# Performance work log

Measured on AMD Instinct MI355X. Metric: run time of the kernel, lower is better.

## Reference

```python
import jax, jax.numpy as jnp
import numpy as np

N_SRC1, N_TGT1, N_TGT2 = 200000, 50000, 10000
E1, E2 = 1000000, 300000
F_IN, F_HID, F_OUT = 256, 192, 128


def setup_inputs() -> dict:
    key = jax.random.key(0)
    ks = jax.random.split(key, 16)
    x = jax.random.normal(ks[0], (N_SRC1, F_IN), dtype=jnp.float32)
    ei1 = jnp.stack([
        jax.random.randint(ks[1], (E1,), 0, N_SRC1, dtype=jnp.int32),
        jax.random.randint(ks[2], (E1,), 0, N_TGT1, dtype=jnp.int32),
    ])
    ei2 = jnp.stack([
        jax.random.randint(ks[3], (E2,), 0, N_TGT1, dtype=jnp.int32),
        jax.random.randint(ks[4], (E2,), 0, N_TGT2, dtype=jnp.int32),
    ])
    def w(k, o, i):
        return jax.random.normal(k, (o, i), dtype=jnp.float32) * (1.0 / np.sqrt(i))
    return {
        "x": x, "ei1": ei1, "ei2": ei2,
        "Wl1": w(ks[5], F_HID, F_IN), "bl1": jnp.zeros((F_HID,), jnp.float32), "Wr1": w(ks[6], F_HID, F_IN),
        "Wl2": w(ks[7], F_HID, F_HID), "bl2": jnp.zeros((F_HID,), jnp.float32), "Wr2": w(ks[8], F_HID, F_HID),
        "W1": w(ks[9], F_HID, F_HID), "b1": jnp.zeros((F_HID,), jnp.float32),
        "W2": w(ks[10], F_OUT, F_HID), "b2": jnp.zeros((F_OUT,), jnp.float32),
    }


def _segment_mean(feat, tgt, n):
    s = jax.ops.segment_sum(feat, tgt, num_segments=n)  # [n, d]
    c = jax.ops.segment_sum(jnp.ones((tgt.shape[0], 1), feat.dtype), tgt, num_segments=n)
    return s / jnp.maximum(c, 1.0)


def _sage_conv(x, ei, n_tgt, Wl, bl, Wr):
    # PyG SAGEConv (mean aggr): lin_l(mean of src feats per tgt) + lin_r(x_target)
    agg = _segment_mean(x[ei[0]], ei[1], n_tgt)
    return agg @ Wl.T + bl + x[:n_tgt] @ Wr.T


def reference(x, ei1, ei2, Wl1, bl1, Wr1, Wl2, bl2, Wr2, W1, b1, W2, b2):
    h = jax.nn.relu(_sage_conv(x, ei1, N_TGT1, Wl1, bl1, Wr1))   # dropout is identity in eval
    h = jax.nn.relu(_sage_conv(h, ei2, N_TGT2, Wl2, bl2, Wr2))
    embedding = h @ W1.T + b1
    h = jax.nn.relu(embedding)
    logits = h @ W2.T + b2
    return jax.nn.log_softmax(logits, axis=-1), embedding
```

## Files before the change

### kernel.cpp

```cpp
#include <hip/hip_runtime.h>
#include <hip/hip_bf16.h>

#define N_SRC1 200000
#define N_TGT1 50000
#define N_TGT2 10000
#define E1_N   1000000
#define E2_N   300000
#define F_IN   256
#define F_HID  192
#define F_OUT  128

typedef __attribute__((ext_vector_type(4))) float f32x4;
typedef __attribute__((ext_vector_type(8))) short short8;

__device__ inline float bf2f(ushort u) {
    union { uint i; float f; } c; c.i = ((uint)u) << 16; return c.f;
}
__device__ inline ushort f2bf(float f) {
    union { float f; uint i; } c; c.f = f;
    uint u = c.i;
    return (ushort)((u + 0x7FFFu + ((u >> 16) & 1u)) >> 16);
}
__device__ inline uint pack2(float a, float b) {
    return (uint)f2bf(a) | ((uint)f2bf(b) << 16);
}

__global__ __launch_bounds__(256) void prep(
    const float4* __restrict__ x4, uint2* __restrict__ xb,
    const float* __restrict__ Wl1, const float* __restrict__ Wr1,
    const float* __restrict__ Wl2, const float* __restrict__ Wr2,
    const float* __restrict__ W1, const float* __restrict__ W2,
    ushort* __restrict__ wc1, ushort* __restrict__ wc2,
    ushort* __restrict__ w1b, ushort* __restrict__ w2b)
{
    const int b = blockIdx.x, tid = threadIdx.x;
    if (b < 2048) {
        const int n4 = N_SRC1 * F_IN / 4;
        for (int i = b * 256 + tid; i < n4; i += 2048 * 256) {
            float4 v = x4[i];
            uint2 o;
            o.x = pack2(v.x, v.y);
            o.y = pack2(v.z, v.w);
            xb[i] = o;
        }
        return;
    }
    const int wt = (b - 2048) * 256 + tid;
    for (int idx = wt; idx < 233472; idx += 128 * 256) {
        if (idx < 98304) {
            int n = idx >> 9, k = idx & 511;
            float v = (k < 256) ? Wl1[n * 256 + k] : Wr1[n * 256 + (k - 256)];
            wc1[idx] = f2bf(v);
        } else if (idx < 98304 + 73728) {
            int i2 = idx - 98304;
            int n = i2 / 384, k = i2 - n * 384;
            float v = (k < 192) ? Wl2[n * 192 + k] : Wr2[n * 192 + (k - 192)];
            wc2[i2] = f2bf(v);
        } else if (idx < 98304 + 73728 + 36864) {
            int i3 = idx - (98304 + 73728);
            w1b[i3] = f2bf(W1[i3]);
        } else {
            int i4 = idx - (98304 + 73728 + 36864);
            w2b[i4] = f2bf(W2[i4]);
        }
    }
}

__global__ __launch_bounds__(256) void hist_kernel(
    const int* __restrict__ tgt, int* __restrict__ cnt, int E)
{
    int i = blockIdx.x * blockDim.x + threadIdx.x;
    if (i < E) atomicAdd(cnt + tgt[i], 1);
}

__global__ __launch_bounds__(256) void scan_blocks(
    const int* __restrict__ cnt, int n, int* __restrict__ off,
    int* __restrict__ partials)
{
    __shared__ int s[256];
    int tid = threadIdx.x;
    int i = blockIdx.x * 256 + tid;
    int v = (i < n) ? cnt[i] : 0;
    s[tid] = v;
    __syncthreads();
#pragma unroll
    for (int o = 1; o < 256; o <<= 1) {
        int t = (tid >= o) ? s[tid - o] : 0;
        __syncthreads();
        s[tid] += t;
        __syncthreads();
    }
    if (i < n) off[i] = s[tid] - v;
    if (tid == 255) partials[blockIdx.x] = s[255];
}

__global__ __launch_bounds__(256) void scan_partials_block(
    int* __restrict__ partials, int np, int* __restrict__ total_out)
{
    __shared__ int s[256];
    int tid = threadIdx.x;
    int v = (tid < np) ? partials[tid] : 0;
    s[tid] = v;
    __syncthreads();
#pragma unroll
    for (int o = 1; o < 256; o <<= 1) {
        int t = (tid >= o) ? s[tid - o] : 0;
        __syncthreads();
        s[tid] += t;
        __syncthreads();
    }
    if (tid < np) partials[tid] = s[tid] - v;
    if (tid == 255) *total_out = s[255];
}

__global__ __launch_bounds__(256) void add_off(
    int* __restrict__ off, const int* __restrict__ partials,
    int* __restrict__ cur, int n)
{
    int i = blockIdx.x * blockDim.x + threadIdx.x;
    if (i < n) {
        int v = off[i] + partials[i >> 8];
        off[i] = v;
        cur[i] = v;
    }
}

__global__ __launch_bounds__(256) void fill_edges(
    const int* __restrict__ src, const int* __restrict__ tgt,
    int* __restrict__ cur, int* __restrict__ esrc, int E)
{
    int i = blockIdx.x * blockDim.x + threadIdx.x;
    if (i < E) {
        int pos = atomicAdd(cur + tgt[i], 1);
        esrc[pos] = src[i];
    }
}

__global__ __launch_bounds__(256) void aggregate_bf16_256(
    const int* __restrict__ esrc, const int* __restrict__ off,
    const ushort* __restrict__ X, ushort* __restrict__ seg, int n)
{
    int wid  = blockIdx.x * 4 + (threadIdx.x >> 6);
    int lane = threadIdx.x & 63;
    if (wid >= n) return;
    int s0 = off[wid], s1 = off[wid + 1];
    float a0 = 0, a1 = 0, a2 = 0, a3 = 0;
    const uint2* base = (const uint2*)X;
    int e = s0;
    for (; e + 4 <= s1; e += 4) {
        int i0 = esrc[e], i1 = esrc[e + 1], i2 = esrc[e + 2], i3 = esrc[e + 3];
        uint2 v0 = base[(size_t)i0 * 64 + lane];
        uint2 v1 = base[(size_t)i1 * 64 + lane];
        uint2 v2 = base[(size_t)i2 * 64 + lane];
        uint2 v3 = base[(size_t)i3 * 64 + lane];
        a0 += bf2f((ushort)(v0.x & 0xffff)) + bf2f((ushort)(v1.x & 0xffff))
            + bf2f((ushort)(v2.x & 0xffff)) + bf2f((ushort)(v3.x & 0xffff));
        a1 += bf2f((ushort)(v0.x >> 16)) + bf2f((ushort)(v1.x >> 16))
            + bf2f((ushort)(v2.x >> 16)) + bf2f((ushort)(v3.x >> 16));
        a2 += bf2f((ushort)(v0.y & 0xffff)) + bf2f((ushort)(v1.y & 0xffff))
            + bf2f((ushort)(v2.y & 0xffff)) + bf2f((ushort)(v3.y & 0xffff));
        a3 += bf2f((ushort)(v0.y >> 16)) + bf2f((ushort)(v1.y >> 16))
            + bf2f((ushort)(v2.y >> 16)) + bf2f((ushort)(v3.y >> 16));
    }
    for (; e < s1; ++e) {
        uint2 v = base[(size_t)esrc[e] * 64 + lane];
        a0 += bf2f((ushort)(v.x & 0xffff)); a1 += bf2f((ushort)(v.x >> 16));
        a2 += bf2f((ushort)(v.y & 0xffff)); a3 += bf2f((ushort)(v.y >> 16));
    }
    float inv = (s1 > s0) ? 1.0f / (float)(s1 - s0) : 0.0f;
    uint2 o;
    o.x = pack2(a0 * inv, a1 * inv);
    o.y = pack2(a2 * inv, a3 * inv);
    ((uint2*)seg)[(size_t)wid * 64 + lane] = o;
}

__global__ __launch_bounds__(256) void aggregate_bf16_192(
    const int* __restrict__ esrc, const int* __restrict__ off,
    const ushort* __restrict__ X, ushort* __restrict__ seg, int n)
{
    int wid  = blockIdx.x * 4 + (threadIdx.x >> 6);
    int lane = threadIdx.x & 63;
    if (wid >= n) return;
    int s0 = off[wid], s1 = off[wid + 1];
    float a0 = 0, a1 = 0, a2 = 0, a3 = 0;
    const uint* base = (const uint*)X;
    int e = s0;
    for (; e + 4 <= s1; e += 4) {
        const uint* r0 = base + (size_t)esrc[e] * 96;
        const uint* r1 = base + (size_t)esrc[e + 1] * 96;
        const uint* r2 = base + (size_t)esrc[e + 2] * 96;
        const uint* r3 = base + (size_t)esrc[e + 3] * 96;
        uint w0 = r0[lane], w1 = r1[lane], w2 = r2[lane], w3 = r3[lane];
        a0 += bf2f((ushort)(w0 & 0xffff)) + bf2f((ushort)(w1 & 0xffff))
            + bf2f((ushort)(w2 & 0xffff)) + bf2f((ushort)(w3 & 0xffff));
        a1 += bf2f((ushort)(w0 >> 16)) + bf2f((ushort)(w1 >> 16))
            + bf2f((ushort)(w2 >> 16)) + bf2f((ushort)(w3 >> 16));
        if (lane < 32) {
            uint u0 = r0[64 + lane], u1 = r1[64 + lane],
                 u2 = r2[64 + lane], u3 = r3[64 + lane];
            a2 += bf2f((ushort)(u0 & 0xffff)) + bf2f((ushort)(u1 & 0xffff))
                + bf2f((ushort)(u2 & 0xffff)) + bf2f((ushort)(u3 & 0xffff));
            a3 += bf2f((ushort)(u0 >> 16)) + bf2f((ushort)(u1 >> 16))
                + bf2f((ushort)(u2 >> 16)) + bf2f((ushort)(u3 >> 16));
        }
    }
    for (; e < s1; ++e) {
        const uint* r = base + (size_t)esrc[e] * 96;
        uint v0 = r[lane];
        a0 += bf2f((ushort)(v0 & 0xffff)); a1 += bf2f((ushort)(v0 >> 16));
        if (lane < 32) {
            uint v1 = r[64 + lane];
            a2 += bf2f((ushort)(v1 & 0xffff)); a3 += bf2f((ushort)(v1 >> 16));
        }
    }
    float inv = (s1 > s0) ? 1.0f / (float)(s1 - s0) : 0.0f;
    uint* o = (uint*)seg + (size_t)wid * 96;
    o[lane] = pack2(a0 * inv, a1 * inv);
    if (lane < 32) o[64 + lane] = pack2(a2 * inv, a3 * inv);
}

template <int BM, int BN, int WM, int WN>
__global__ __launch_bounds__(WM * WN * 64) void gemm_mfma(
    const ushort* __restrict__ A1, int K1,
    const ushort* __restrict__ A2, int K2,
    const ushort* __restrict__ W, const float* __restrict__ bias,
    ushort* __restrict__ Cb, float* __restrict__ Cf,
    int M, int relu)
{
    constexpr int TPB = WM * WN * 64;
    constexpr int WTM = BM / WM, WTN = BN / WN;
    constexpr int MF = WTM / 16, NF = WTN / 16;
    constexpr int ROW = 40;
    __shared__ __attribute__((aligned(16))) ushort As[BM * ROW];
    __shared__ __attribute__((aligned(16))) ushort Ws[BN * ROW];
    const int tid  = threadIdx.x;
    const int lane = tid & 63;
    const int wid  = tid >> 6;
    const int wm = wid / WN, wn = wid % WN;
    const int bm = blockIdx.x * BM;
    const int K = K1 + K2;

    f32x4 acc[MF][NF];
#pragma unroll
    for (int i = 0; i < MF; ++i)
#pragma unroll
        for (int j = 0; j < NF; ++j) acc[i][j] = {0.f, 0.f, 0.f, 0.f};

    for (int k0 = 0; k0 < K; k0 += 32) {
#pragma unroll
        for (int c = tid; c < BM * 4; c += TPB) {
            int row = c >> 2, k8 = (c & 3) * 8;
            int m = bm + row, k = k0 + k8;
            uint4 v = make_uint4(0, 0, 0, 0);
            if (m < M) {
                const ushort* s = (k < K1) ? (A1 + (size_t)m * K1 + k)
                                           : (A2 + (size_t)m * K2 + (k - K1));
                v = *(const uint4*)s;
            }
            *(uint4*)&As[row * ROW + k8] = v;
        }
#pragma unroll
        for (int c = tid; c < BN * 4; c += TPB) {
            int row = c >> 2, k8 = (c & 3) * 8;
            uint4 v = *(const uint4*)(W + (size_t)row * K + k0 + k8);
            *(uint4*)&Ws[row * ROW + k8] = v;
        }
        __syncthreads();
        short8 a[MF], b[NF];
#pragma unroll
        for (int mf = 0; mf < MF; ++mf)
            a[mf] = *(const short8*)&As[(wm * WTM + mf * 16 + (lane & 15)) * ROW + (lane >> 4) * 8];
#pragma unroll
        for (int nf = 0; nf < NF; ++nf)
            b[nf] = *(const short8*)&Ws[(wn * WTN + nf * 16 + (lane & 15)) * ROW + (lane >> 4) * 8];
#pragma unroll
        for (int mf = 0; mf < MF; ++mf)
#pragma unroll
            for (int nf = 0; nf < NF; ++nf)
                acc[mf][nf] = __builtin_amdgcn_mfma_f32_16x16x32_bf16(
                    a[mf], b[nf], acc[mf][nf], 0, 0, 0);
        __syncthreads();
    }

#pragma unroll
    for (int mf = 0; mf < MF; ++mf) {
        int r0 = bm + wm * WTM + mf * 16 + (lane >> 4) * 4;
#pragma unroll
        for (int nf = 0; nf < NF; ++nf) {
            int cc = wn * WTN + nf * 16 + (lane & 15);
            float bi = bias[cc];
#pragma unroll
            for (int r = 0; r < 4; ++r) {
                int m = r0 + r;
                if (m >= M) continue;
                float v = acc[mf][nf][r] + bi;
                if (Cf) Cf[(size_t)m * BN + cc] = v;
                if (Cb) Cb[(size_t)m * BN + cc] = f2bf(relu ? fmaxf(v, 0.f) : v);
            }
        }
    }
}

__global__ __launch_bounds__(256) void logsoftmax128(
    const float* __restrict__ logits, float* __restrict__ out, int M)
{
    long long gid = (long long)blockIdx.x * blockDim.x + threadIdx.x;
    int row  = (int)(gid >> 6);
    int lane = (int)(gid & 63);
    if (row >= M) return;
    const float* r = logits + (size_t)row * 128;
    float a = r[lane], b = r[lane + 64];
    float mx = fmaxf(a, b);
#pragma unroll
    for (int o = 32; o > 0; o >>= 1) mx = fmaxf(mx, __shfl_xor(mx, o));
    float s = expf(a - mx) + expf(b - mx);
#pragma unroll
    for (int o = 32; o > 0; o >>= 1) s += __shfl_xor(s, o);
    float ls = logf(s) + mx;
    out[(size_t)row * 128 + lane]      = a - ls;
    out[(size_t)row * 128 + lane + 64] = b - ls;
}

extern "C" void kernel_launch(void* const* d_in, const int* in_sizes, int n_in,
                              void* d_out, int out_size, void* d_ws, size_t ws_size,
                              hipStream_t stream)
{
    const float* x   = (const float*)d_in[0];
    const int*   ei1 = (const int*)d_in[1];
    const int*   ei2 = (const int*)d_in[2];
    const float* Wl1 = (const float*)d_in[3];
    const float* bl1 = (const float*)d_in[4];
    const float* Wr1 = (const float*)d_in[5];
    const float* Wl2 = (const float*)d_in[6];
    const float* bl2 = (const float*)d_in[7];
    const float* Wr2 = (const float*)d_in[8];
    const float* W1  = (const float*)d_in[9];
    const float* b1  = (const float*)d_in[10];
    const float* W2  = (const float*)d_in[11];
    const float* b2  = (const float*)d_in[12];

    char* ws = (char*)d_ws;
    ushort* xb    = (ushort*)(ws + 0);
    ushort* seg1b = (ushort*)(ws + 102400000);
    ushort* h1b   = (ushort*)(ws + 128000000);
    int*    esrc1 = (int*)   (ws + 147200000);
    int*    cnt1  = (int*)   (ws + 151200000);
    int*    off1  = (int*)   (ws + 151400000);
    int*    part  = (int*)   (ws + 151600064);
    ushort* wc1   = (ushort*)(ws + 151601152);
    ushort* wc2   = (ushort*)(ws + 151797760);
    ushort* w1b   = (ushort*)(ws + 151945216);
    ushort* w2b   = (ushort*)(ws + 152018944);
    ushort* seg2b = (ushort*)(ws + 152068096);
    int*    esrc2 = (int*)   (ws + 147200000);
    int*    cnt2  = (int*)   (ws + 148400000);
    int*    off2  = (int*)   (ws + 148440064);
    ushort* h2b    = (ushort*)(ws + 102400000);
    ushort* h3b    = (ushort*)(ws + 106240000);
    float*  logits = (float*) (ws + 110080000);

    float* out_ls  = (float*)d_out;
    float* out_emb = (float*)d_out + (size_t)N_TGT2 * F_OUT;

    const int NP1 = (N_TGT1 + 255) / 256;
    const int NP2 = (N_TGT2 + 255) / 256;

    prep<<<2176, 256, 0, stream>>>(
        (const float4*)x, (uint2*)xb, Wl1, Wr1, Wl2, Wr2, W1, W2,
        wc1, wc2, w1b, w2b);

    hipMemsetAsync(cnt1, 0, 200000, stream);
    hist_kernel<<<(E1_N + 255) / 256, 256, 0, stream>>>(ei1 + E1_N, cnt1, E1_N);
    scan_blocks<<<NP1, 256, 0, stream>>>(cnt1, N_TGT1, off1, part);
    scan_partials_block<<<1, 256, 0, stream>>>(part, NP1, off1 + N_TGT1);
    add_off<<<NP1, 256, 0, stream>>>(off1, part, cnt1 , N_TGT1);
    fill_edges<<<(E1_N + 255) / 256, 256, 0, stream>>>(ei1, ei1 + E1_N, cnt1, esrc1, E1_N);
    aggregate_bf16_256<<<(N_TGT1 + 3) / 4, 256, 0, stream>>>(esrc1, off1, xb, seg1b, N_TGT1);

    gemm_mfma<128, 192, 4, 2><<<(N_TGT1 + 127) / 128, 512, 0, stream>>>(
        seg1b, F_IN, xb, F_IN, wc1, bl1, h1b, nullptr, N_TGT1, 1);

    hipMemsetAsync(cnt2, 0, 40000, stream);
    hist_kernel<<<(E2_N + 255) / 256, 256, 0, stream>>>(ei2 + E2_N, cnt2, E2_N);
    scan_blocks<<<NP2, 256, 0, stream>>>(cnt2, N_TGT2, off2, part);
    scan_partials_block<<<1, 256, 0, stream>>>(part, NP2, off2 + N_TGT2);
    add_off<<<NP2, 256, 0, stream>>>(off2, part, cnt2 , N_TGT2);
    fill_edges<<<(E2_N + 255) / 256, 256, 0, stream>>>(ei2, ei2 + E2_N, cnt2, esrc2, E2_N);
    aggregate_bf16_192<<<(N_TGT2 + 3) / 4, 256, 0, stream>>>(esrc2, off2, h1b, seg2b, N_TGT2);

    gemm_mfma<64, 192, 4, 2><<<(N_TGT2 + 63) / 64, 512, 0, stream>>>(
        seg2b, F_HID, h1b, F_HID, wc2, bl2, h2b, nullptr, N_TGT2, 1);

    gemm_mfma<64, 192, 4, 2><<<(N_TGT2 + 63) / 64, 512, 0, stream>>>(
        h2b, F_HID, nullptr, 0, w1b, b1, h3b, out_emb, N_TGT2, 1);

    gemm_mfma<64, 128, 4, 2><<<(N_TGT2 + 63) / 64, 512, 0, stream>>>(
        h3b, F_HID, nullptr, 0, w2b, b2, nullptr, logits, N_TGT2, 0);

    logsoftmax128<<<(N_TGT2 * 64 + 255) / 256, 256, 0, stream>>>(logits, out_ls, N_TGT2);
}
```

Before: 396.5 us.

## Fuse histograms into prep, single-block scans, fuse tail GEMMs with log-softmax

Both edge histograms now run inside the prep kernel. The multi-kernel prefix scans are replaced by one 1024-thread scan kernel per layer. The layer-2 SAGE GEMM, the embedding GEMM, the output GEMM and log-softmax are fused into one kernel that keeps the intermediates in LDS. The aggregation loop is unrolled to 8 gathers, and the layer-1 GEMM tile changes to 64x192 with a 2x4 wave grid. Together these remove about ten launches and the global round-trips of the tail intermediates. The costs are a single-block serial scan and a tail kernel with large LDS use and low occupancy.

```diff
diff --git a/kernel.cpp b/kernel.cpp
--- a/kernel.cpp
+++ b/kernel.cpp
@@ -25,13 +25,18 @@
     return (uint)f2bf(a) | ((uint)f2bf(b) << 16);
 }
 
+#define HB1 3907
+#define HB2 1172
+
 __global__ __launch_bounds__(256) void prep(
     const float4* __restrict__ x4, uint2* __restrict__ xb,
     const float* __restrict__ Wl1, const float* __restrict__ Wr1,
     const float* __restrict__ Wl2, const float* __restrict__ Wr2,
     const float* __restrict__ W1, const float* __restrict__ W2,
     ushort* __restrict__ wc1, ushort* __restrict__ wc2,
-    ushort* __restrict__ w1b, ushort* __restrict__ w2b)
+    ushort* __restrict__ w1b, ushort* __restrict__ w2b,
+    const int* __restrict__ tgt1, const int* __restrict__ tgt2,
+    int* __restrict__ cnt1, int* __restrict__ cnt2)
 {
     const int b = blockIdx.x, tid = threadIdx.x;
     if (b < 2048) {
@@ -45,84 +50,65 @@
         }
         return;
     }
-    const int wt = (b - 2048) * 256 + tid;
-    for (int idx = wt; idx < 233472; idx += 128 * 256) {
-        if (idx < 98304) {
-            int n = idx >> 9, k = idx & 511;
-            float v = (k < 256) ? Wl1[n * 256 + k] : Wr1[n * 256 + (k - 256)];
-            wc1[idx] = f2bf(v);
-        } else if (idx < 98304 + 73728) {
-            int i2 = idx - 98304;
-            int n = i2 / 384, k = i2 - n * 384;
-            float v = (k < 192) ? Wl2[n * 192 + k] : Wr2[n * 192 + (k - 192)];
-            wc2[i2] = f2bf(v);
-        } else if (idx < 98304 + 73728 + 36864) {
-            int i3 = idx - (98304 + 73728);
-            w1b[i3] = f2bf(W1[i3]);
-        } else {
-            int i4 = idx - (98304 + 73728 + 36864);
-            w2b[i4] = f2bf(W2[i4]);
-        }
-    }
-}
-
-__global__ __launch_bounds__(256) void hist_kernel(
-    const int* __restrict__ tgt, int* __restrict__ cnt, int E)
-{
-    int i = blockIdx.x * blockDim.x + threadIdx.x;
-    if (i < E) atomicAdd(cnt + tgt[i], 1);
-}
-
-__global__ __launch_bounds__(256) void scan_blocks(
-    const int* __restrict__ cnt, int n, int* __restrict__ off,
-    int* __restrict__ partials)
-{
-    __shared__ int s[256];
-    int tid = threadIdx.x;
-    int i = blockIdx.x * 256 + tid;
-    int v = (i < n) ? cnt[i] : 0;
-    s[tid] = v;
+    if (b < 2176) {
+        const int wt = (b - 2048) * 256 + tid;
+        for (int idx = wt; idx < 233472; idx += 128 * 256) {
+            if (idx < 98304) {
+                int n = idx >> 9, k = idx & 511;
+                float v = (k < 256) ? Wl1[n * 256 + k] : Wr1[n * 256 + (k - 256)];
+                wc1[idx] = f2bf(v);
+            } else if (idx < 98304 + 73728) {
+                int i2 = idx - 98304;
+                int n = i2 / 384, k = i2 - n * 384;
+                float v = (k < 192) ? Wl2[n * 192 + k] : Wr2[n * 192 + (k - 192)];
+                wc2[i2] = f2bf(v);
+            } else if (idx < 98304 + 73728 + 36864) {
+                int i3 = idx - (98304 + 73728);
+                w1b[i3] = f2bf(W1[i3]);
+            } else {
+                int i4 = idx - (98304 + 73728 + 36864);
+                w2b[i4] = f2bf(W2[i4]);
+            }
+        }
+        return;
+    }
+    if (b < 2176 + HB1) {
+        int e = (b - 2176) * 256 + tid;
+        if (e < E1_N) atomicAdd(cnt1 + tgt1[e], 1);
+        return;
+    }
+    int e = (b - 2176 - HB1) * 256 + tid;
+    if (e < E2_N) atomicAdd(cnt2 + tgt2[e], 1);
+}
+
+__global__ __launch_bounds__(1024) void scan_full(
+    int* __restrict__ cnt, int n, int* __restrict__ off)
+{
+    __shared__ int s[1024];
+    const int tid = threadIdx.x;
+    const int chunk = (n + 1023) >> 10;
+    int lo = tid * chunk, hi = lo + chunk;
+    if (lo > n) lo = n;
+    if (hi > n) hi = n;
+    int sum = 0;
+    for (int i = lo; i < hi; ++i) sum += cnt[i];
+    s[tid] = sum;
     __syncthreads();
 #pragma unroll
-    for (int o = 1; o < 256; o <<= 1) {
+    for (int o = 1; o < 1024; o <<= 1) {
         int t = (tid >= o) ? s[tid - o] : 0;
         __syncthreads();
         s[tid] += t;
         __syncthreads();
     }
-    if (i < n) off[i] = s[tid] - v;
-    if (tid == 255) partials[blockIdx.x] = s[255];
-}
-
-__global__ __launch_bounds__(256) void scan_partials_block(
-    int* __restrict__ partials, int np, int* __restrict__ total_out)
-{
-    __shared__ int s[256];
-    int tid = threadIdx.x;
-    int v = (tid < np) ? partials[tid] : 0;
-    s[tid] = v;
-    __syncthreads();
-#pragma unroll
-    for (int o = 1; o < 256; o <<= 1) {
-        int t = (tid >= o) ? s[tid - o] : 0;
-        __syncthreads();
-        s[tid] += t;
-        __syncthreads();
-    }
-    if (tid < np) partials[tid] = s[tid] - v;
-    if (tid == 255) *total_out = s[255];
-}
-
-__global__ __launch_bounds__(256) void add_off(
-    int* __restrict__ off, const int* __restrict__ partials,
-    int* __restrict__ cur, int n)
-{
-    int i = blockIdx.x * blockDim.x + threadIdx.x;
-    if (i < n) {
-        int v = off[i] + partials[i >> 8];
-        off[i] = v;
-        cur[i] = v;
-    }
+    int run = s[tid] - sum;
+    for (int i = lo; i < hi; ++i) {
+        int v = cnt[i];
+        off[i] = run;
+        cnt[i] = run;
+        run += v;
+    }
+    if (tid == 1023) off[n] = s[1023];
 }
 
 __global__ __launch_bounds__(256) void fill_edges(
@@ -147,20 +133,18 @@
     float a0 = 0, a1 = 0, a2 = 0, a3 = 0;
     const uint2* base = (const uint2*)X;
     int e = s0;
-    for (; e + 4 <= s1; e += 4) {
-        int i0 = esrc[e], i1 = esrc[e + 1], i2 = esrc[e + 2], i3 = esrc[e + 3];
-        uint2 v0 = base[(size_t)i0 * 64 + lane];
-        uint2 v1 = base[(size_t)i1 * 64 + lane];
-        uint2 v2 = base[(size_t)i2 * 64 + lane];
-        uint2 v3 = base[(size_t)i3 * 64 + lane];
-        a0 += bf2f((ushort)(v0.x & 0xffff)) + bf2f((ushort)(v1.x & 0xffff))
-            + bf2f((ushort)(v2.x & 0xffff)) + bf2f((ushort)(v3.x & 0xffff));
-        a1 += bf2f((ushort)(v0.x >> 16)) + bf2f((ushort)(v1.x >> 16))
-            + bf2f((ushort)(v2.x >> 16)) + bf2f((ushort)(v3.x >> 16));
-        a2 += bf2f((ushort)(v0.y & 0xffff)) + bf2f((ushort)(v1.y & 0xffff))
-            + bf2f((ushort)(v2.y & 0xffff)) + bf2f((ushort)(v3.y & 0xffff));
-        a3 += bf2f((ushort)(v0.y >> 16)) + bf2f((ushort)(v1.y >> 16))
-            + bf2f((ushort)(v2.y >> 16)) + bf2f((ushort)(v3.y >> 16));
+    for (; e + 8 <= s1; e += 8) {
+        uint2 v[8];
+#pragma unroll
+        for (int j = 0; j < 8; ++j)
+            v[j] = base[(size_t)esrc[e + j] * 64 + lane];
+#pragma unroll
+        for (int j = 0; j < 8; ++j) {
+            a0 += bf2f((ushort)(v[j].x & 0xffff));
+            a1 += bf2f((ushort)(v[j].x >> 16));
+            a2 += bf2f((ushort)(v[j].y & 0xffff));
+            a3 += bf2f((ushort)(v[j].y >> 16));
+        }
     }
     for (; e < s1; ++e) {
         uint2 v = base[(size_t)esrc[e] * 64 + lane];
@@ -224,8 +208,7 @@
     const ushort* __restrict__ A1, int K1,
     const ushort* __restrict__ A2, int K2,
     const ushort* __restrict__ W, const float* __restrict__ bias,
-    ushort* __restrict__ Cb, float* __restrict__ Cf,
-    int M, int relu)
+    ushort* __restrict__ Cb, int M, int relu)
 {
     constexpr int TPB = WM * WN * 64;
     constexpr int WTM = BM / WM, WTN = BN / WN;
@@ -294,31 +277,158 @@
                 int m = r0 + r;
                 if (m >= M) continue;
                 float v = acc[mf][nf][r] + bi;
-                if (Cf) Cf[(size_t)m * BN + cc] = v;
-                if (Cb) Cb[(size_t)m * BN + cc] = f2bf(relu ? fmaxf(v, 0.f) : v);
-            }
-        }
-    }
-}
-
-__global__ __launch_bounds__(256) void logsoftmax128(
-    const float* __restrict__ logits, float* __restrict__ out, int M)
-{
-    long long gid = (long long)blockIdx.x * blockDim.x + threadIdx.x;
-    int row  = (int)(gid >> 6);
-    int lane = (int)(gid & 63);
-    if (row >= M) return;
-    const float* r = logits + (size_t)row * 128;
-    float a = r[lane], b = r[lane + 64];
-    float mx = fmaxf(a, b);
-#pragma unroll
-    for (int o = 32; o > 0; o >>= 1) mx = fmaxf(mx, __shfl_xor(mx, o));
-    float s = expf(a - mx) + expf(b - mx);
-#pragma unroll
-    for (int o = 32; o > 0; o >>= 1) s += __shfl_xor(s, o);
-    float ls = logf(s) + mx;
-    out[(size_t)row * 128 + lane]      = a - ls;
-    out[(size_t)row * 128 + lane + 64] = b - ls;
+                Cb[(size_t)m * BN + cc] = f2bf(relu ? fmaxf(v, 0.f) : v);
+            }
+        }
+    }
+}
+
+__global__ __launch_bounds__(512) void tail_fused(
+    const ushort* __restrict__ seg2, const ushort* __restrict__ h1,
+    const ushort* __restrict__ wc2, const float* __restrict__ bl2,
+    const ushort* __restrict__ w1b, const float* __restrict__ b1,
+    const ushort* __restrict__ w2b, const float* __restrict__ b2,
+    float* __restrict__ out_emb, float* __restrict__ out_ls, int M)
+{
+    __shared__ __attribute__((aligned(16))) char lds[122880];
+    ushort* As0   = (ushort*)lds;
+    ushort* Ws0   = (ushort*)(lds + 5120);
+    ushort* h2buf = (ushort*)(lds + 20480);
+    ushort* h3buf = (ushort*)(lds + 46080);
+    ushort* w2buf = (ushort*)(lds + 71680);
+    float*  lsbuf = (float*)(lds + 71680);
+
+    const int tid = threadIdx.x, lane = tid & 63, wid = tid >> 6;
+    const int wm = wid >> 1, wn = wid & 1;
+    const int bm = blockIdx.x * 64;
+
+    for (int c = tid; c < 128 * 24; c += 512) {
+        int r = c / 24, k8 = (c % 24) * 8;
+        uint4 v = *(const uint4*)(w2b + r * 192 + k8);
+        *(uint4*)&w2buf[r * 200 + k8] = v;
+    }
+
+    {
+        f32x4 acc[6];
+#pragma unroll
+        for (int j = 0; j < 6; ++j) acc[j] = {0.f, 0.f, 0.f, 0.f};
+        for (int k0 = 0; k0 < 384; k0 += 32) {
+            if (tid < 256) {
+                int row = tid >> 2, k8 = (tid & 3) * 8;
+                int m = bm + row, k = k0 + k8;
+                uint4 v = make_uint4(0, 0, 0, 0);
+                if (m < M) {
+                    const ushort* s = (k < 192) ? (seg2 + (size_t)m * 192 + k)
+                                                : (h1 + (size_t)m * 192 + (k - 192));
+                    v = *(const uint4*)s;
+                }
+                *(uint4*)&As0[row * 40 + k8] = v;
+            }
+            for (int c = tid; c < 768; c += 512) {
+                int row = c >> 2, k8 = (c & 3) * 8;
+                uint4 v = *(const uint4*)(wc2 + (size_t)row * 384 + k0 + k8);
+                *(uint4*)&Ws0[row * 40 + k8] = v;
+            }
+            __syncthreads();
+            short8 a = *(const short8*)&As0[(wm * 16 + (lane & 15)) * 40 + (lane >> 4) * 8];
+#pragma unroll
+            for (int nf = 0; nf < 6; ++nf) {
+                short8 b = *(const short8*)&Ws0[(wn * 96 + nf * 16 + (lane & 15)) * 40 + (lane >> 4) * 8];
+                acc[nf] = __builtin_amdgcn_mfma_f32_16x16x32_bf16(a, b, acc[nf], 0, 0, 0);
+            }
+            __syncthreads();
+        }
+#pragma unroll
+        for (int nf = 0; nf < 6; ++nf) {
+            int cc = wn * 96 + nf * 16 + (lane & 15);
+            float bi = bl2[cc];
+#pragma unroll
+            for (int r = 0; r < 4; ++r) {
+                int row = wm * 16 + (lane >> 4) * 4 + r;
+                h2buf[row * 200 + cc] = f2bf(fmaxf(acc[nf][r] + bi, 0.f));
+            }
+        }
+    }
+    __syncthreads();
+
+    {
+        f32x4 acc[6];
+#pragma unroll
+        for (int j = 0; j < 6; ++j) acc[j] = {0.f, 0.f, 0.f, 0.f};
+        for (int k0 = 0; k0 < 192; k0 += 32) {
+            for (int c = tid; c < 768; c += 512) {
+                int row = c >> 2, k8 = (c & 3) * 8;
+                uint4 v = *(const uint4*)(w1b + (size_t)row * 192 + k0 + k8);
+                *(uint4*)&Ws0[row * 40 + k8] = v;
+            }
+            __syncthreads();
+            short8 a = *(const short8*)&h2buf[(wm * 16 + (lane & 15)) * 200 + k0 + (lane >> 4) * 8];
+#pragma unroll
+            for (int nf = 0; nf < 6; ++nf) {
+                short8 b = *(const short8*)&Ws0[(wn * 96 + nf * 16 + (lane & 15)) * 40 + (lane >> 4) * 8];
+                acc[nf] = __builtin_amdgcn_mfma_f32_16x16x32_bf16(a, b, acc[nf], 0, 0, 0);
+            }
+            __syncthreads();
+        }
+#pragma unroll
+        for (int nf = 0; nf < 6; ++nf) {
+            int cc = wn * 96 + nf * 16 + (lane & 15);
+            float bi = b1[cc];
+#pragma unroll
+            for (int r = 0; r < 4; ++r) {
+                int row = wm * 16 + (lane >> 4) * 4 + r;
+                int m = bm + row;
+                float v = acc[nf][r] + bi;
+                if (m < M) out_emb[(size_t)m * 192 + cc] = v;
+                h3buf[row * 200 + cc] = f2bf(fmaxf(v, 0.f));
+            }
+        }
+    }
+    __syncthreads();
+
+    {
+        f32x4 acc[4];
+#pragma unroll
+        for (int j = 0; j < 4; ++j) acc[j] = {0.f, 0.f, 0.f, 0.f};
+#pragma unroll
+        for (int k0 = 0; k0 < 192; k0 += 32) {
+            short8 a = *(const short8*)&h3buf[(wm * 16 + (lane & 15)) * 200 + k0 + (lane >> 4) * 8];
+#pragma unroll
+            for (int nf = 0; nf < 4; ++nf) {
+                short8 b = *(const short8*)&w2buf[(wn * 64 + nf * 16 + (lane & 15)) * 200 + k0 + (lane >> 4) * 8];
+                acc[nf] = __builtin_amdgcn_mfma_f32_16x16x32_bf16(a, b, acc[nf], 0, 0, 0);
+            }
+        }
+        __syncthreads();
+#pragma unroll
+        for (int nf = 0; nf < 4; ++nf) {
+            int cc = wn * 64 + nf * 16 + (lane & 15);
+            float bi = b2[cc];
+#pragma unroll
+            for (int r = 0; r < 4; ++r) {
+                int row = wm * 16 + (lane >> 4) * 4 + r;
+                lsbuf[row * 128 + cc] = acc[nf][r] + bi;
+            }
+        }
+    }
+    __syncthreads();
+
+    for (int i = 0; i < 8; ++i) {
+        int row = wid * 8 + i;
+        float a = lsbuf[row * 128 + lane], b = lsbuf[row * 128 + 64 + lane];
+        float mx = fmaxf(a, b);
+#pragma unroll
+        for (int o = 32; o > 0; o >>= 1) mx = fmaxf(mx, __shfl_xor(mx, o));
+        float s = expf(a - mx) + expf(b - mx);
+#pragma unroll
+        for (int o = 32; o > 0; o >>= 1) s += __shfl_xor(s, o);
+        float ls = logf(s) + mx;
+        int m = bm + row;
+        if (m < M) {
+            out_ls[(size_t)m * 128 + lane]      = a - ls;
+            out_ls[(size_t)m * 128 + lane + 64] = b - ls;
+        }
+    }
 }
 
 extern "C" void kernel_launch(void* const* d_in, const int* in_sizes, int n_in,
@@ -345,57 +455,36 @@
     ushort* h1b   = (ushort*)(ws + 128000000);
     int*    esrc1 = (int*)   (ws + 147200000);
     int*    cnt1  = (int*)   (ws + 151200000);
-    int*    off1  = (int*)   (ws + 151400000);
-    int*    part  = (int*)   (ws + 151600064);
-    ushort* wc1   = (ushort*)(ws + 151601152);
-    ushort* wc2   = (ushort*)(ws + 151797760);
-    ushort* w1b   = (ushort*)(ws + 151945216);
-    ushort* w2b   = (ushort*)(ws + 152018944);
-    ushort* seg2b = (ushort*)(ws + 152068096);
-    int*    esrc2 = (int*)   (ws + 147200000);
-    int*    cnt2  = (int*)   (ws + 148400000);
-    int*    off2  = (int*)   (ws + 148440064);
-    ushort* h2b    = (ushort*)(ws + 102400000);
-    ushort* h3b    = (ushort*)(ws + 106240000);
-    float*  logits = (float*) (ws + 110080000);
+    int*    cnt2  = (int*)   (ws + 151400000);
+    int*    off1  = (int*)   (ws + 151440000);
+    int*    off2  = (int*)   (ws + 151640064);
+    ushort* wc1   = (ushort*)(ws + 151680128);
+    ushort* wc2   = (ushort*)(ws + 151876736);
+    ushort* w1b   = (ushort*)(ws + 152024192);
+    ushort* w2b   = (ushort*)(ws + 152097920);
+    ushort* seg2b = (ushort*)(ws + 152147072);
+    int*    esrc2 = (int*)   (ws + 155987072);
 
     float* out_ls  = (float*)d_out;
     float* out_emb = (float*)d_out + (size_t)N_TGT2 * F_OUT;
 
-    const int NP1 = (N_TGT1 + 255) / 256;
-    const int NP2 = (N_TGT2 + 255) / 256;
-
-    prep<<<2176, 256, 0, stream>>>(
+    hipMemsetAsync(cnt1, 0, 240000, stream);
+
+    prep<<<2176 + HB1 + HB2, 256, 0, stream>>>(
         (const float4*)x, (uint2*)xb, Wl1, Wr1, Wl2, Wr2, W1, W2,
-        wc1, wc2, w1b, w2b);
-
-    hipMemsetAsync(cnt1, 0, 200000, stream);
-    hist_kernel<<<(E1_N + 255) / 256, 256, 0, stream>>>(ei1 + E1_N, cnt1, E1_N);
-    scan_blocks<<<NP1, 256, 0, stream>>>(cnt1, N_TGT1, off1, part);
-    scan_partials_block<<<1, 256, 0, stream>>>(part, NP1, off1 + N_TGT1);
-    add_off<<<NP1, 256, 0, stream>>>(off1, part, cnt1 , N_TGT1);
-    fill_edges<<<(E1_N + 255) / 256, 256, 0, stream>>>(ei1, ei1 + E1_N, cnt1, esrc1, E1_N);
+        wc1, wc2, w1b, w2b, ei1 + E1_N, ei2 + E2_N, cnt1, cnt2);
+
+    scan_full<<<1, 1024, 0, stream>>>(cnt1, N_TGT1, off1);
+    fill_edges<<<HB1, 256, 0, stream>>>(ei1, ei1 + E1_N, cnt1, esrc1, E1_N);
+    scan_full<<<1, 1024, 0, stream>>>(cnt2, N_TGT2, off2);
+    fill_edges<<<HB2, 256, 0, stream>>>(ei2, ei2 + E2_N, cnt2, esrc2, E2_N);
+
     aggregate_bf16_256<<<(N_TGT1 + 3) / 4, 256, 0, stream>>>(esrc1, off1, xb, seg1b, N_TGT1);
-
-    gemm_mfma<128, 192, 4, 2><<<(N_TGT1 + 127) / 128, 512, 0, stream>>>(
-        seg1b, F_IN, xb, F_IN, wc1, bl1, h1b, nullptr, N_TGT1, 1);
-
-    hipMemsetAsync(cnt2, 0, 40000, stream);
-    hist_kernel<<<(E2_N + 255) / 256, 256, 0, stream>>>(ei2 + E2_N, cnt2, E2_N);
-    scan_blocks<<<NP2, 256, 0, stream>>>(cnt2, N_TGT2, off2, part);
-    scan_partials_block<<<1, 256, 0, stream>>>(part, NP2, off2 + N_TGT2);
-    add_off<<<NP2, 256, 0, stream>>>(off2, part, cnt2 , N_TGT2);
-    fill_edges<<<(E2_N + 255) / 256, 256, 0, stream>>>(ei2, ei2 + E2_N, cnt2, esrc2, E2_N);
+    gemm_mfma<64, 192, 2, 4><<<(N_TGT1 + 63) / 64, 512, 0, stream>>>(
+        seg1b, F_IN, xb, F_IN, wc1, bl1, h1b, N_TGT1, 1);
+
     aggregate_bf16_192<<<(N_TGT2 + 3) / 4, 256, 0, stream>>>(esrc2, off2, h1b, seg2b, N_TGT2);
 
-    gemm_mfma<64, 192, 4, 2><<<(N_TGT2 + 63) / 64, 512, 0, stream>>>(
-        seg2b, F_HID, h1b, F_HID, wc2, bl2, h2b, nullptr, N_TGT2, 1);
-
-    gemm_mfma<64, 192, 4, 2><<<(N_TGT2 + 63) / 64, 512, 0, stream>>>(
-        h2b, F_HID, nullptr, 0, w1b, b1, h3b, out_emb, N_TGT2, 1);
-
-    gemm_mfma<64, 128, 4, 2><<<(N_TGT2 + 63) / 64, 512, 0, stream>>>(
-        h3b, F_HID, nullptr, 0, w2b, b2, nullptr, logits, N_TGT2, 0);
-
-    logsoftmax128<<<(N_TGT2 * 64 + 255) / 256, 256, 0, stream>>>(logits, out_ls, N_TGT2);
-}
+    tail_fused<<<(N_TGT2 + 63) / 64, 512, 0, stream>>>(
+        seg2b, h1b, wc2, bl2, w1b, b1, w2b, b2, out_emb, out_ls, N_TGT2);
+}
```

Measured after the change: 465.2 us. +17.3%, slower.
